# Performance work log

Measured on AMD Instinct MI355X. Metric: run time of the kernel, lower is better.

Reference implementation:

```python
import jax, jax.numpy as jnp
import numpy as np

B, C, H, W = 1024, 10, 30, 30


def setup_inputs() -> dict:
    key = jax.random.key(0)
    k1, k2, k3 = jax.random.split(key, 3)
    pred = jax.random.normal(k1, (B, C, H, W), dtype=jnp.float32)
    target = jax.random.normal(k2, (B, C, H, W), dtype=jnp.float32)
    input_grid = jax.random.normal(k3, (B, C, H, W), dtype=jnp.float32)
    return {"pred": pred, "target": target, "input_grid": input_grid}


def reference(pred, target, input_grid):
    dt = pred.dtype
    n_colors = pred.shape[1]
    pred_idx = jnp.argmax(pred, axis=1)      # [B,H,W]
    tgt_idx = jnp.argmax(target, axis=1)     # [B,H,W]
    inp_idx = jnp.argmax(input_grid, axis=1)  # [B,H,W]

    logp = jax.nn.log_softmax(pred, axis=1)  # [B,C,H,W]
    ce = -jnp.take_along_axis(logp, tgt_idx[:, None], axis=1)[:, 0]  # [B,H,W]
    incorrect = (pred_idx != tgt_idx).astype(dt)
    ce_loss = jnp.mean(ce * (1.0 + 4.0 * incorrect))

    exact_matches = jnp.all(pred_idx == tgt_idx, axis=(1, 2)).astype(dt)  # [B]
    exact_bonus = -1.0 * jnp.mean(exact_matches)

    should_not_copy = jnp.any(tgt_idx != inp_idx, axis=(1, 2)).astype(dt)
    did_copy = jnp.all(pred_idx == inp_idx, axis=(1, 2)).astype(dt)
    copy_penalty = 5.0 * jnp.mean(should_not_copy * did_copy)

    changed_pixels = jnp.mean((pred_idx != inp_idx).astype(dt), axis=(1, 2))  # [B]
    target_changed = jnp.mean((tgt_idx != inp_idx).astype(dt), axis=(1, 2))
    transform_diff = jnp.mean((changed_pixels - target_changed) ** 2)

    # color-set penalty (GPU-native replacement of per-batch unique/CPU loop):
    # a color is "present" iff any pixel has that index; missing = in target set but not pred set
    colors = jnp.arange(n_colors)
    pred_present = jnp.any(pred_idx[..., None] == colors, axis=(1, 2))  # [B,C] bool
    tgt_present = jnp.any(tgt_idx[..., None] == colors, axis=(1, 2))    # [B,C] bool
    missing = jnp.sum(tgt_present & jnp.logical_not(pred_present)).astype(dt)
    color_penalty = 0.1 * missing

    total = ce_loss + exact_bonus + copy_penalty + transform_diff + color_penalty
    total = jnp.where(jnp.isnan(total), jnp.asarray(2.0, dt),
                      jnp.where(total > 100.0, jnp.asarray(10.0, dt), total))
    return (total, ce_loss, copy_penalty, -exact_bonus, jnp.sum(exact_matches), transform_diff)
```

## Files before the change

kernel.cpp:

```cpp
#include <hip/hip_runtime.h>
#include <math.h>

constexpr int BATCH = 1024;
constexpr int NC    = 10;
constexpr int HW    = 900;
constexpr int PPB   = 225;

__global__ __launch_bounds__(256, 4) void loss_main(
    const float* __restrict__ pred, const float* __restrict__ target,
    const float* __restrict__ inp, float4* __restrict__ ws) {
  const int img  = blockIdx.x >> 2;
  const int part = blockIdx.x & 3;
  const int t    = threadIdx.x;

  float ce_sum = 0.f;
  unsigned combo = 0;
  int counts = 0;

  if (t < PPB) {
    const int q = part * PPB + t;
    const size_t base = (size_t)img * NC * HW + q;

    float p[NC], tv[NC], gv[NC];
#pragma unroll
    for (int c = 0; c < NC; ++c) p[c]  = pred[base + c * HW];
#pragma unroll
    for (int c = 0; c < NC; ++c) tv[c] = target[base + c * HW];
#pragma unroll
    for (int c = 0; c < NC; ++c) gv[c] = inp[base + c * HW];

    float pmax = p[0]; int pidx = 0;
#pragma unroll
    for (int c = 1; c < NC; ++c)
      if (p[c] > pmax) { pmax = p[c]; pidx = c; }

    float s = 0.f;
#pragma unroll
    for (int c = 0; c < NC; ++c) s += __expf(p[c] - pmax);
    const float lse = pmax + __logf(s);

    float tmax = tv[0]; int tidx = 0;
#pragma unroll
    for (int c = 1; c < NC; ++c)
      if (tv[c] > tmax) { tmax = tv[c]; tidx = c; }
    float gmax = gv[0]; int gidx = 0;
#pragma unroll
    for (int c = 1; c < NC; ++c)
      if (gv[c] > gmax) { gmax = gv[c]; gidx = c; }

    float ptv = p[0];
#pragma unroll
    for (int c = 1; c < NC; ++c)
      if (tidx == c) ptv = p[c];

    const float ce = lse - ptv;
    const float w  = (pidx != tidx) ? 5.0f : 1.0f;
    ce_sum = ce * w;
    combo  = (1u << pidx) | (1u << (10 + tidx));
    if (pidx != tidx) combo |= 1u << 20;
    if (tidx != gidx) combo |= 1u << 21;
    if (pidx != gidx) combo |= 1u << 22;
    counts = ((pidx != gidx) ? 1 : 0) | ((tidx != gidx) ? (1 << 16) : 0);
  }

#pragma unroll
  for (int off = 32; off >= 1; off >>= 1) {
    ce_sum += __shfl_down(ce_sum, off);
    combo  |= __shfl_down(combo, off);
    counts += __shfl_down(counts, off);
  }

  __shared__ float s_ce[4];
  __shared__ unsigned s_or[4];
  __shared__ int s_cnt[4];
  const int wave = t >> 6;
  if ((t & 63) == 0) { s_ce[wave] = ce_sum; s_or[wave] = combo; s_cnt[wave] = counts; }
  __syncthreads();
  if (t == 0) {
    float4 slot;
    slot.x = s_ce[0] + s_ce[1] + s_ce[2] + s_ce[3];
    slot.y = __uint_as_float(s_or[0] | s_or[1] | s_or[2] | s_or[3]);
    slot.z = __int_as_float(s_cnt[0] + s_cnt[1] + s_cnt[2] + s_cnt[3]);
    slot.w = 0.f;
    ws[blockIdx.x] = slot;
  }
}

__global__ __launch_bounds__(1024) void loss_final(
    const float4* __restrict__ ws, float* __restrict__ out) {
  const int b = threadIdx.x;

  float ce = 0.f; unsigned orv = 0; int cnt = 0;
#pragma unroll
  for (int k = 0; k < 4; ++k) {
    const float4 v = ws[b * 4 + k];
    ce  += v.x;
    orv |= __float_as_uint(v.y);
    cnt += __float_as_int(v.z);
  }
  const int changed  = cnt & 0xFFFF;
  const int tchanged = cnt >> 16;
  const float exact   = (orv & (1u << 20)) ? 0.f : 1.f;
  const float any_ti  = (orv & (1u << 21)) ? 1.f : 0.f;
  const float all_pi  = (orv & (1u << 22)) ? 0.f : 1.f;
  const unsigned pm = orv & 0x3FFu, tm = (orv >> 10) & 0x3FFu;
  const float d = (float)(changed - tchanged) * (1.0f / (float)HW);

  float r_ce   = ce;
  float r_ex   = exact;
  float r_cp   = any_ti * all_pi;
  float r_td   = d * d;
  float r_mi   = (float)__popc(tm & ~pm);

#pragma unroll
  for (int off = 32; off >= 1; off >>= 1) {
    r_ce += __shfl_down(r_ce, off);
    r_ex += __shfl_down(r_ex, off);
    r_cp += __shfl_down(r_cp, off);
    r_td += __shfl_down(r_td, off);
    r_mi += __shfl_down(r_mi, off);
  }

  __shared__ float red[16][5];
  const int wave = b >> 6;
  if ((b & 63) == 0) {
    red[wave][0] = r_ce; red[wave][1] = r_ex; red[wave][2] = r_cp;
    red[wave][3] = r_td; red[wave][4] = r_mi;
  }
  __syncthreads();
  if (b == 0) {
    float a0 = 0, a1 = 0, a2 = 0, a3 = 0, a4 = 0;
#pragma unroll
    for (int w = 0; w < 16; ++w) {
      a0 += red[w][0]; a1 += red[w][1]; a2 += red[w][2];
      a3 += red[w][3]; a4 += red[w][4];
    }
    const float ce_loss    = a0 * (1.0f / ((float)BATCH * (float)HW));
    const float exact_sum  = a1;
    const float exact_frac = exact_sum * (1.0f / (float)BATCH);
    const float copy_pen   = 5.0f * a2 * (1.0f / (float)BATCH);
    const float tdiff      = a3 * (1.0f / (float)BATCH);
    const float color_pen  = 0.1f * a4;
    float total = ce_loss - exact_frac + copy_pen + tdiff + color_pen;
    if (isnan(total)) total = 2.0f;
    else if (total > 100.0f) total = 10.0f;
    out[0] = total;
    out[1] = ce_loss;
    out[2] = copy_pen;
    out[3] = exact_frac;
    out[4] = exact_sum;
    out[5] = tdiff;
  }
}

extern "C" void kernel_launch(void* const* d_in, const int* in_sizes, int n_in,
                              void* d_out, int out_size, void* d_ws, size_t ws_size,
                              hipStream_t stream) {
  const float* pred   = (const float*)d_in[0];
  const float* target = (const float*)d_in[1];
  const float* inp    = (const float*)d_in[2];
  float4* ws = (float4*)d_ws;
  loss_main<<<dim3(BATCH * 4), dim3(256), 0, stream>>>(pred, target, inp, ws);
  loss_final<<<dim3(1), dim3(1024), 0, stream>>>(ws, (float*)d_out);
}
```

Measured before the change: 131.5 us.

## Use float4 loads with four pixels per thread and one block per image

Each thread now loads float4 vectors and handles four adjacent pixels, so one 225-thread block covers a whole image instead of four blocks per image. The first kernel writes one workspace slot per image, and the final kernel reads one slot per thread instead of four. The aim is wider memory transactions, fewer blocks and a smaller reduction. In exchange, register use per thread rises (120 floats live) and only 1024 blocks are launched, which may lower occupancy and reduce latency hiding.

```diff
diff --git a/kernel.cpp b/kernel.cpp
--- a/kernel.cpp
+++ b/kernel.cpp
@@ -4,63 +4,92 @@
 constexpr int BATCH = 1024;
 constexpr int NC    = 10;
 constexpr int HW    = 900;
-constexpr int PPB   = 225;
+constexpr int NQ    = 225;
+
+union F4 { float4 v; float f[4]; };
 
 __global__ __launch_bounds__(256, 4) void loss_main(
     const float* __restrict__ pred, const float* __restrict__ target,
     const float* __restrict__ inp, float4* __restrict__ ws) {
-  const int img  = blockIdx.x >> 2;
-  const int part = blockIdx.x & 3;
-  const int t    = threadIdx.x;
+  const int img = blockIdx.x;
+  const int t   = threadIdx.x;
 
   float ce_sum = 0.f;
   unsigned combo = 0;
   int counts = 0;
 
-  if (t < PPB) {
-    const int q = part * PPB + t;
-    const size_t base = (size_t)img * NC * HW + q;
+  if (t < NQ) {
+    const size_t base = (size_t)img * (NC * HW) + 4 * t;
 
-    float p[NC], tv[NC], gv[NC];
+    F4 tv[NC], gv[NC];
 #pragma unroll
-    for (int c = 0; c < NC; ++c) p[c]  = pred[base + c * HW];
+    for (int c = 0; c < NC; ++c)
+      tv[c].v = *reinterpret_cast<const float4*>(target + base + c * HW);
 #pragma unroll
-    for (int c = 0; c < NC; ++c) tv[c] = target[base + c * HW];
+    for (int c = 0; c < NC; ++c)
+      gv[c].v = *reinterpret_cast<const float4*>(inp + base + c * HW);
+
+    float tmax[4], gmax[4];
+    int tidx[4], gidx[4];
 #pragma unroll
-    for (int c = 0; c < NC; ++c) gv[c] = inp[base + c * HW];
+    for (int k = 0; k < 4; ++k) {
+      tmax[k] = tv[0].f[k]; tidx[k] = 0;
+      gmax[k] = gv[0].f[k]; gidx[k] = 0;
+    }
+#pragma unroll
+    for (int c = 1; c < NC; ++c) {
+#pragma unroll
+      for (int k = 0; k < 4; ++k) {
+        if (tv[c].f[k] > tmax[k]) { tmax[k] = tv[c].f[k]; tidx[k] = c; }
+        if (gv[c].f[k] > gmax[k]) { gmax[k] = gv[c].f[k]; gidx[k] = c; }
+      }
+    }
 
-    float pmax = p[0]; int pidx = 0;
+    F4 p[NC];
 #pragma unroll
-    for (int c = 1; c < NC; ++c)
-      if (p[c] > pmax) { pmax = p[c]; pidx = c; }
+    for (int c = 0; c < NC; ++c)
+      p[c].v = *reinterpret_cast<const float4*>(pred + base + c * HW);
 
-    float s = 0.f;
+    float pmax[4]; int pidx[4];
 #pragma unroll
-    for (int c = 0; c < NC; ++c) s += __expf(p[c] - pmax);
-    const float lse = pmax + __logf(s);
+    for (int k = 0; k < 4; ++k) { pmax[k] = p[0].f[k]; pidx[k] = 0; }
+#pragma unroll
+    for (int c = 1; c < NC; ++c) {
+#pragma unroll
+      for (int k = 0; k < 4; ++k)
+        if (p[c].f[k] > pmax[k]) { pmax[k] = p[c].f[k]; pidx[k] = c; }
+    }
 
-    float tmax = tv[0]; int tidx = 0;
+    float s[4] = {0.f, 0.f, 0.f, 0.f};
 #pragma unroll
-    for (int c = 1; c < NC; ++c)
-      if (tv[c] > tmax) { tmax = tv[c]; tidx = c; }
-    float gmax = gv[0]; int gidx = 0;
+    for (int c = 0; c < NC; ++c) {
 #pragma unroll
-    for (int c = 1; c < NC; ++c)
-      if (gv[c] > gmax) { gmax = gv[c]; gidx = c; }
+      for (int k = 0; k < 4; ++k)
+        s[k] += __expf(p[c].f[k] - pmax[k]);
+    }
 
-    float ptv = p[0];
+    float ptv[4];
 #pragma unroll
-    for (int c = 1; c < NC; ++c)
-      if (tidx == c) ptv = p[c];
+    for (int k = 0; k < 4; ++k) ptv[k] = p[0].f[k];
+#pragma unroll
+    for (int c = 1; c < NC; ++c) {
+#pragma unroll
+      for (int k = 0; k < 4; ++k)
+        if (tidx[k] == c) ptv[k] = p[c].f[k];
+    }
 
-    const float ce = lse - ptv;
-    const float w  = (pidx != tidx) ? 5.0f : 1.0f;
-    ce_sum = ce * w;
-    combo  = (1u << pidx) | (1u << (10 + tidx));
-    if (pidx != tidx) combo |= 1u << 20;
-    if (tidx != gidx) combo |= 1u << 21;
-    if (pidx != gidx) combo |= 1u << 22;
-    counts = ((pidx != gidx) ? 1 : 0) | ((tidx != gidx) ? (1 << 16) : 0);
+#pragma unroll
+    for (int k = 0; k < 4; ++k) {
+      const float lse = pmax[k] + __logf(s[k]);
+      const float ce  = lse - ptv[k];
+      ce_sum += ce * ((pidx[k] != tidx[k]) ? 5.0f : 1.0f);
+      combo |= (1u << pidx[k]) | (1u << (10 + tidx[k]));
+      if (pidx[k] != tidx[k]) combo |= 1u << 20;
+      if (tidx[k] != gidx[k]) combo |= 1u << 21;
+      if (pidx[k] != gidx[k]) combo |= 1u << 22;
+      counts += ((pidx[k] != gidx[k]) ? 1 : 0) +
+                ((tidx[k] != gidx[k]) ? (1 << 16) : 0);
+    }
   }
 
 #pragma unroll
@@ -82,7 +111,7 @@
     slot.y = __uint_as_float(s_or[0] | s_or[1] | s_or[2] | s_or[3]);
     slot.z = __int_as_float(s_cnt[0] + s_cnt[1] + s_cnt[2] + s_cnt[3]);
     slot.w = 0.f;
-    ws[blockIdx.x] = slot;
+    ws[img] = slot;
   }
 }
 
@@ -90,14 +119,11 @@
     const float4* __restrict__ ws, float* __restrict__ out) {
   const int b = threadIdx.x;
 
-  float ce = 0.f; unsigned orv = 0; int cnt = 0;
-#pragma unroll
-  for (int k = 0; k < 4; ++k) {
-    const float4 v = ws[b * 4 + k];
-    ce  += v.x;
-    orv |= __float_as_uint(v.y);
-    cnt += __float_as_int(v.z);
-  }
+  const float4 v = ws[b];
+  const float ce = v.x;
+  const unsigned orv = __float_as_uint(v.y);
+  const int cnt = __float_as_int(v.z);
+
   const int changed  = cnt & 0xFFFF;
   const int tchanged = cnt >> 16;
   const float exact   = (orv & (1u << 20)) ? 0.f : 1.f;
@@ -160,6 +186,6 @@
   const float* target = (const float*)d_in[1];
   const float* inp    = (const float*)d_in[2];
   float4* ws = (float4*)d_ws;
-  loss_main<<<dim3(BATCH * 4), dim3(256), 0, stream>>>(pred, target, inp, ws);
+  loss_main<<<dim3(BATCH), dim3(256), 0, stream>>>(pred, target, inp, ws);
   loss_final<<<dim3(1), dim3(1024), 0, stream>>>(ws, (float*)d_out);
 }
```

Measured after the change: 133.0 us. About the same (+1.1%).
